# Performance work log

Hardware: AMD Instinct MI355X
Metric: run time of the kernel (lower is better)

Reference implementation:

```python
import jax, jax.numpy as jnp
import numpy as np

BS, NC, Nc, D_n = 8, 256, 128, 64
ALPHA, HS, HM = 2, 256, 128
GAMMA_MAX = 0.5
EPS = 1e-6


def setup_inputs() -> dict:
    key = jax.random.key(0)
    ks = jax.random.split(key, 12)
    f = jax.random.normal
    return {
        "x": f(ks[0], (BS, NC, D_n), jnp.float32),
        "h": f(ks[1], (BS, NC, Nc, D_n), jnp.float32) * 0.1,
        "W": f(ks[2], (BS, NC, Nc, Nc), jnp.float32) * (Nc ** -0.5),
        "decay": jax.random.uniform(ks[3], (BS, NC, Nc), jnp.float32),
        "hebbian": f(ks[4], (BS, NC, Nc, Nc), jnp.float32) * 0.01,
        "neuron_id": f(ks[5], (NC, Nc, D_n), jnp.float32) * (D_n ** -0.5),
        "state_w1": f(ks[6], (HS, 2 * D_n), jnp.float32) * ((2 * D_n) ** -0.5),
        "state_b1": jnp.zeros((HS,), jnp.float32),
        "state_w2": f(ks[7], (D_n, HS), jnp.float32) * (HS ** -0.5),
        "state_b2": jnp.zeros((D_n,), jnp.float32),
        "msg_w1": f(ks[8], (HM, D_n), jnp.float32) * (D_n ** -0.5),
        "msg_b1": jnp.zeros((HM,), jnp.float32),
        "msg_w2": f(ks[9], (D_n, HM), jnp.float32) * (HM ** -0.5),
        "msg_b2": jnp.zeros((D_n,), jnp.float32),
        "inject_w": f(ks[10], (NC, ALPHA * D_n, D_n), jnp.float32) * (D_n ** -0.5),
        "inject_b": jnp.zeros((NC, ALPHA * D_n), jnp.float32),
        "W_decay_logit": jnp.full((NC, Nc), -3.0, jnp.float32),
        "decay_gamma_logit": jnp.full((NC, Nc), -3.0, jnp.float32),
        "hebbian_decay_logit": jnp.full((NC, Nc), 2.0, jnp.float32),
    }


def _rms_norm(v):
    # F.rms_norm over the last (Nc) axis, no affine weight
    return v * jax.lax.rsqrt(jnp.mean(v * v, axis=-1, keepdims=True) + EPS)


def reference(x, h, W, decay, hebbian, neuron_id,
              state_w1, state_b1, state_w2, state_b2,
              msg_w1, msg_b1, msg_w2, msg_b2,
              inject_w, inject_b,
              W_decay_logit, decay_gamma_logit, hebbian_decay_logit):
    B = x.shape[0]
    # per-cell injection of external input into the first ALPHA neurons
    inj = jnp.einsum('bcd,cad->bca', x, inject_w) + inject_b   # [B,NC,ALPHA*D_n]
    h = h.at[:, :, :ALPHA, :].add(inj.reshape(B, NC, ALPHA, D_n))
    h_id = h + neuron_id                                       # identity embedding broadcast
    # per-neuron message MLP (tanh hidden)
    m = jnp.tanh(jnp.einsum('bcnd,hd->bcnh', h_id, msg_w1) + msg_b1)
    m = jnp.einsum('bcnh,dh->bcnd', m, msg_w2) + msg_b2        # [B,NC,Nc,D_n]
    # Hebbian-weighted adjacency message passing: small per-cell matmul W @ m
    agg = jnp.einsum('bcij,bcjd->bcid', W, m)
    # state update MLP on concat(state, aggregated message)
    s = jnp.tanh(jnp.einsum('bcnd,hd->bcnh',
                            jnp.concatenate([h_id, agg], axis=-1), state_w1) + state_b1)
    dh = jnp.einsum('bcnh,dh->bcnd', s, state_w2) + state_b2
    # gated decay of per-neuron state
    dg = GAMMA_MAX * jax.nn.sigmoid(decay_gamma_logit)         # [NC,Nc]
    decay_new = (1.0 - dg) * decay + dg * jax.nn.sigmoid(jnp.mean(dh, axis=-1))
    h_new = (1.0 - decay_new[..., None]) * h + decay_new[..., None] * jnp.tanh(dh)
    # Hebbian outer-product plasticity
    hg = GAMMA_MAX * jax.nn.sigmoid(hebbian_decay_logit)
    outer = jnp.einsum('bcid,bcjd->bcij', h_new, m) / D_n
    hebbian_new = (1.0 - hg[..., None]) * hebbian + hg[..., None] * outer
    # decayed adjacency update + rms-norm over the incoming-edge axis
    wg = GAMMA_MAX * jax.nn.sigmoid(W_decay_logit)
    W_new = _rms_norm((1.0 - wg[..., None]) * W + wg[..., None] * hebbian_new)
    return (h_new, m, W_new, decay_new, hebbian_new)
```

## Files before the change

### kernel.cpp

```cpp
#include <hip/hip_runtime.h>


#define NCELL 256

typedef __attribute__((ext_vector_type(8))) short bf16x8;
typedef __attribute__((ext_vector_type(4))) float f32x4;
typedef __attribute__((ext_vector_type(4))) unsigned short u16x4;

#define MFMA(a, b, c) __builtin_amdgcn_mfma_f32_16x16x32_bf16((a), (b), (c), 0, 0, 0)

__device__ __forceinline__ unsigned short f2bf(float f) {
    unsigned u = __builtin_bit_cast(unsigned, f);
    u = (u + 0x7FFFu + ((u >> 16) & 1u)) >> 16;
    return (unsigned short)u;
}
__device__ __forceinline__ float frcp(float x) { return __builtin_amdgcn_rcpf(x); }
__device__ __forceinline__ float sigm(float v) { return frcp(1.0f + __expf(-v)); }
__device__ __forceinline__ float ftanh(float x) {
    float e = __expf(2.0f * x);
    return 1.0f - 2.0f * frcp(e + 1.0f);
}

__device__ __forceinline__ int sw64(int row, int col) {
    return row * 64 + ((((col >> 3) ^ row) & 7) << 3) + (col & 7);
}
__device__ __forceinline__ int sw128(int row, int col) {
    return row * 128 + (((col >> 3) ^ (row & 7)) << 3) + (col & 7);
}
__device__ __forceinline__ int sw32(int row, int col) {
    return row * 32 + ((((col >> 3) ^ row) & 3) << 3) + (col & 7);
}

__global__ void cvt_w(const float* __restrict__ a, const float* __restrict__ b,
                      const float* __restrict__ c, const float* __restrict__ d,
                      unsigned short* __restrict__ dst) {
    int i = blockIdx.x * 256 + threadIdx.x;
    float v;
    if (i < 8192) v = a[i];
    else if (i < 16384) v = b[i - 8192];
    else if (i < 49152) v = c[i - 16384];
    else v = d[i - 49152];
    dst[i] = f2bf(v);
}

__global__ __launch_bounds__(256, 4)
void cell_kernel(const float* __restrict__ x, const float* __restrict__ h,
                 const float* __restrict__ W, const float* __restrict__ decay,
                 const float* __restrict__ nid,
                 const float* __restrict__ sb1, const float* __restrict__ sb2,
                 const float* __restrict__ mb1, const float* __restrict__ mb2,
                 const float* __restrict__ injw, const float* __restrict__ injb,
                 const float* __restrict__ dgl,
                 const unsigned short* __restrict__ wbf,
                 float* __restrict__ out) {
    const int cell = blockIdx.x;
    const int c = cell & (NCELL - 1);
    const int tid = threadIdx.x;
    const int wv = tid >> 6;
    const int lane = tid & 63;
    const int lr = lane & 15;
    const int lg = lane >> 4;

    float* out_h = out;
    float* out_m = out + 16777216;
    float* out_d = out + 67108864;

    const unsigned short* w1m = wbf;
    const unsigned short* w2m = wbf + 8192;
    const unsigned short* w1s = wbf + 16384;
    const unsigned short* w2s = wbf + 49152;

    __shared__ alignas(16) unsigned char smem[33280];
    unsigned short* mT_s = (unsigned short*)smem;
    unsigned short* st_s = (unsigned short*)(smem + 16384);
    float* inj_s = (float*)(smem + 32768);
    unsigned short* hbuf = st_s + wv * 2048;

    float4 wpa[4][2][2];
    {
        const float* Wbase = W + (size_t)cell * 16384;
        #pragma unroll
        for (int ks = 0; ks < 4; ++ks)
            #pragma unroll
            for (int rt = 0; rt < 2; ++rt) {
                const float* wr = Wbase + (wv * 32 + rt * 16 + lr) * 128 + ks * 32 + lg * 8;
                wpa[ks][rt][0] = *(const float4*)wr;
                wpa[ks][rt][1] = *(const float4*)(wr + 4);
            }
    }

    if (wv == 0) {
        const float* xr = x + cell * 64;
        const float* i0 = injw + (c * 128 + lane) * 64;
        const float* i1 = i0 + 64 * 64;
        float acc0 = injb[c * 128 + lane];
        float acc1 = injb[c * 128 + 64 + lane];
        #pragma unroll
        for (int d4 = 0; d4 < 16; ++d4) {
            float4 xv = ((const float4*)xr)[d4];
            float4 a = ((const float4*)i0)[d4];
            float4 b = ((const float4*)i1)[d4];
            acc0 += a.x * xv.x + a.y * xv.y + a.z * xv.z + a.w * xv.w;
            acc1 += b.x * xv.x + b.y * xv.y + b.z * xv.z + b.w * xv.w;
        }
        inj_s[lane] = acc0;
        inj_s[64 + lane] = acc1;
    }

    bf16x8 aH[2][2];
    #pragma unroll
    for (int rt = 0; rt < 2; ++rt)
        #pragma unroll
        for (int ks = 0; ks < 2; ++ks) {
            const int row = wv * 32 + rt * 16 + lr;
            const int col = ks * 32 + lg * 8;
            const float* hr = h + (size_t)(cell * 128 + row) * 64 + col;
            const float* nr = nid + (size_t)(c * 128 + row) * 64 + col;
            float4 a0 = *(const float4*)hr;
            float4 a1 = *(const float4*)(hr + 4);
            float4 n0 = *(const float4*)nr;
            float4 n1 = *(const float4*)(nr + 4);
            float v[8] = {a0.x, a0.y, a0.z, a0.w, a1.x, a1.y, a1.z, a1.w};
            float nn[8] = {n0.x, n0.y, n0.z, n0.w, n1.x, n1.y, n1.z, n1.w};
            unsigned short us[8];
            #pragma unroll
            for (int j = 0; j < 8; ++j) {
                float hv = v[j] + nn[j];
                if (row < 2) hv += inj_s[row * 64 + col + j];
                us[j] = f2bf(hv);
            }
            aH[rt][ks] = *(bf16x8*)us;
        }

    f32x4 accM[2][4];
    #pragma unroll
    for (int rt = 0; rt < 2; ++rt)
        #pragma unroll
        for (int dt = 0; dt < 4; ++dt)
            accM[rt][dt] = (f32x4){0.f, 0.f, 0.f, 0.f};

    #pragma unroll
    for (int ch = 0; ch < 4; ++ch) {
        f32x4 accH[2][2];
        #pragma unroll
        for (int rt = 0; rt < 2; ++rt)
            #pragma unroll
            for (int ht = 0; ht < 2; ++ht)
                accH[rt][ht] = (f32x4){0.f, 0.f, 0.f, 0.f};
        #pragma unroll
        for (int ks = 0; ks < 2; ++ks)
            #pragma unroll
            for (int ht = 0; ht < 2; ++ht) {
                bf16x8 bw = *(const bf16x8*)&w1m[(ch * 32 + ht * 16 + lr) * 64 + ks * 32 + lg * 8];
                #pragma unroll
                for (int rt = 0; rt < 2; ++rt)
                    accH[rt][ht] = MFMA(aH[rt][ks], bw, accH[rt][ht]);
            }
        #pragma unroll
        for (int rt = 0; rt < 2; ++rt)
            #pragma unroll
            for (int ht = 0; ht < 2; ++ht) {
                float b1v = mb1[ch * 32 + ht * 16 + lr];
                #pragma unroll
                for (int r = 0; r < 4; ++r) {
                    float t = ftanh(accH[rt][ht][r] + b1v);
                    hbuf[sw32(rt * 16 + lg * 4 + r, ht * 16 + lr)] = f2bf(t);
                }
            }
        #pragma unroll
        for (int rt = 0; rt < 2; ++rt) {
            bf16x8 aM = *(const bf16x8*)&hbuf[sw32(rt * 16 + lr, lg * 8)];
            #pragma unroll
            for (int dt = 0; dt < 4; ++dt) {
                bf16x8 bw = *(const bf16x8*)&w2m[(dt * 16 + lr) * 128 + ch * 32 + lg * 8];
                accM[rt][dt] = MFMA(aM, bw, accM[rt][dt]);
            }
        }
    }
    #pragma unroll
    for (int rt = 0; rt < 2; ++rt)
        #pragma unroll
        for (int dt = 0; dt < 4; ++dt) {
            float b2v = mb2[dt * 16 + lr];
            #pragma unroll
            for (int r = 0; r < 4; ++r) {
                float mv = accM[rt][dt][r] + b2v;
                int n = wv * 32 + rt * 16 + lg * 4 + r;
                int dcol = dt * 16 + lr;
                out_m[(size_t)(cell * 128 + n) * 64 + dcol] = mv;
                mT_s[sw128(dcol, n)] = f2bf(mv);
            }
        }
    __syncthreads();

    f32x4 accA[2][4];
    #pragma unroll
    for (int rt = 0; rt < 2; ++rt)
        #pragma unroll
        for (int dt = 0; dt < 4; ++dt)
            accA[rt][dt] = (f32x4){0.f, 0.f, 0.f, 0.f};
    #pragma unroll
    for (int ks = 0; ks < 4; ++ks)
        #pragma unroll
        for (int rt = 0; rt < 2; ++rt) {
            float4 wa = wpa[ks][rt][0];
            float4 wb = wpa[ks][rt][1];
            unsigned short uw[8] = {f2bf(wa.x), f2bf(wa.y), f2bf(wa.z), f2bf(wa.w),
                                    f2bf(wb.x), f2bf(wb.y), f2bf(wb.z), f2bf(wb.w)};
            bf16x8 aW = *(bf16x8*)uw;
            #pragma unroll
            for (int dt = 0; dt < 4; ++dt) {
                bf16x8 bm = *(const bf16x8*)&mT_s[sw128(dt * 16 + lr, ks * 32 + lg * 8)];
                accA[rt][dt] = MFMA(aW, bm, accA[rt][dt]);
            }
        }
    #pragma unroll
    for (int rt = 0; rt < 2; ++rt)
        #pragma unroll
        for (int dt = 0; dt < 4; ++dt)
            #pragma unroll
            for (int r = 0; r < 4; ++r)
                st_s[sw64(wv * 32 + rt * 16 + lg * 4 + r, dt * 16 + lr)] = f2bf(accA[rt][dt][r]);

    bf16x8 aG[2][2];
    #pragma unroll
    for (int rt = 0; rt < 2; ++rt)
        #pragma unroll
        for (int ks = 0; ks < 2; ++ks)
            aG[rt][ks] = *(const bf16x8*)&st_s[sw64(wv * 32 + rt * 16 + lr, ks * 32 + lg * 8)];

    f32x4 accD[2][4];
    #pragma unroll
    for (int rt = 0; rt < 2; ++rt)
        #pragma unroll
        for (int dt = 0; dt < 4; ++dt)
            accD[rt][dt] = (f32x4){0.f, 0.f, 0.f, 0.f};

    #pragma unroll
    for (int ch = 0; ch < 8; ++ch) {
        f32x4 accS[2][2];
        #pragma unroll
        for (int rt = 0; rt < 2; ++rt)
            #pragma unroll
            for (int ht = 0; ht < 2; ++ht)
                accS[rt][ht] = (f32x4){0.f, 0.f, 0.f, 0.f};
        #pragma unroll
        for (int ks = 0; ks < 4; ++ks)
            #pragma unroll
            for (int ht = 0; ht < 2; ++ht) {
                bf16x8 bw = *(const bf16x8*)&w1s[(ch * 32 + ht * 16 + lr) * 128 + ks * 32 + lg * 8];
                #pragma unroll
                for (int rt = 0; rt < 2; ++rt) {
                    bf16x8 af = (ks < 2) ? aH[rt][ks] : aG[rt][ks - 2];
                    accS[rt][ht] = MFMA(af, bw, accS[rt][ht]);
                }
            }
        #pragma unroll
        for (int rt = 0; rt < 2; ++rt)
            #pragma unroll
            for (int ht = 0; ht < 2; ++ht) {
                float bv = sb1[ch * 32 + ht * 16 + lr];
                #pragma unroll
                for (int r = 0; r < 4; ++r) {
                    float t = ftanh(accS[rt][ht][r] + bv);
                    hbuf[sw32(rt * 16 + lg * 4 + r, ht * 16 + lr)] = f2bf(t);
                }
            }
        #pragma unroll
        for (int rt = 0; rt < 2; ++rt) {
            bf16x8 aS = *(const bf16x8*)&hbuf[sw32(rt * 16 + lr, lg * 8)];
            #pragma unroll
            for (int dt = 0; dt < 4; ++dt) {
                bf16x8 bw = *(const bf16x8*)&w2s[(dt * 16 + lr) * 256 + ch * 32 + lg * 8];
                accD[rt][dt] = MFMA(aS, bw, accD[rt][dt]);
            }
        }
    }

    float dnew_r[2][4];
    #pragma unroll
    for (int rt = 0; rt < 2; ++rt)
        #pragma unroll
        for (int r = 0; r < 4; ++r) {
            float s = 0.f;
            #pragma unroll
            for (int dt = 0; dt < 4; ++dt) {
                accD[rt][dt][r] += sb2[dt * 16 + lr];
                s += accD[rt][dt][r];
            }
            s += __shfl_xor(s, 1);
            s += __shfl_xor(s, 2);
            s += __shfl_xor(s, 4);
            s += __shfl_xor(s, 8);
            int row = wv * 32 + rt * 16 + lg * 4 + r;
            float mean = s * (1.0f / 64.0f);
            float dg = 0.5f * sigm(dgl[c * 128 + row]);
            float dn = (1.0f - dg) * decay[cell * 128 + row] + dg * sigm(mean);
            if (lr == 0) out_d[cell * 128 + row] = dn;
            dnew_r[rt][r] = dn;
        }
    #pragma unroll
    for (int rt = 0; rt < 2; ++rt)
        #pragma unroll
        for (int r = 0; r < 4; ++r) {
            int row = wv * 32 + rt * 16 + lg * 4 + r;
            float dn = dnew_r[rt][r];
            const float* hr = h + (size_t)(cell * 128 + row) * 64;
            #pragma unroll
            for (int dt = 0; dt < 4; ++dt) {
                int col = dt * 16 + lr;
                float hpost = hr[col];
                if (row < 2) hpost += inj_s[row * 64 + col];
                float hn = (1.0f - dn) * hpost + dn * ftanh(accD[rt][dt][r]);
                out_h[(size_t)(cell * 128 + row) * 64 + col] = hn;
            }
        }
}

__global__ __launch_bounds__(256, 4)
void hebb_kernel(const float* __restrict__ W, const float* __restrict__ hebb,
                 const float* __restrict__ wdl, const float* __restrict__ hdl,
                 float* __restrict__ out) {
    const int cell = blockIdx.x;
    const int c = cell & (NCELL - 1);
    const int tid = threadIdx.x;
    const int wv = tid >> 6;
    const int lane = tid & 63;
    const int lr = lane & 15;
    const int lg = lane >> 4;

    const float* hsrc = out + (size_t)cell * 8192;
    const float* msrc = out + 16777216 + (size_t)cell * 8192;
    float* out_W  = out + 33554432;
    float* out_hb = out + 67371008;

    __shared__ alignas(16) unsigned char smem[32768];
    unsigned short* hA = (unsigned short*)smem;
    unsigned short* mB = (unsigned short*)(smem + 16384);

    #pragma unroll
    for (int g = 0; g < 8; ++g) {
        int idx = g * 1024 + tid * 4;
        int row = idx >> 6, col = idx & 63;
        float4 hv = *(const float4*)(hsrc + idx);
        float4 mv = *(const float4*)(msrc + idx);
        u16x4 hu = {f2bf(hv.x), f2bf(hv.y), f2bf(hv.z), f2bf(hv.w)};
        u16x4 mu = {f2bf(mv.x), f2bf(mv.y), f2bf(mv.z), f2bf(mv.w)};
        *(u16x4*)&hA[sw64(row, col)] = hu;
        *(u16x4*)&mB[sw64(row, col)] = mu;
    }
    __syncthreads();

    bf16x8 aO[2][2];
    #pragma unroll
    for (int rt = 0; rt < 2; ++rt)
        #pragma unroll
        for (int ks = 0; ks < 2; ++ks)
            aO[rt][ks] = *(const bf16x8*)&hA[sw64(wv * 32 + rt * 16 + lr, ks * 32 + lg * 8)];

    f32x4 accO[2][8];
    #pragma unroll
    for (int rt = 0; rt < 2; ++rt)
        #pragma unroll
        for (int jt = 0; jt < 8; ++jt)
            accO[rt][jt] = (f32x4){0.f, 0.f, 0.f, 0.f};
    #pragma unroll
    for (int jt = 0; jt < 8; ++jt)
        #pragma unroll
        for (int ks = 0; ks < 2; ++ks) {
            bf16x8 bm = *(const bf16x8*)&mB[sw64(jt * 16 + lr, ks * 32 + lg * 8)];
            #pragma unroll
            for (int rt = 0; rt < 2; ++rt)
                accO[rt][jt] = MFMA(aO[rt][ks], bm, accO[rt][jt]);
        }

    #pragma unroll
    for (int rt = 0; rt < 2; ++rt)
        #pragma unroll
        for (int r = 0; r < 4; ++r) {
            int i = wv * 32 + rt * 16 + lg * 4 + r;
            float hg = 0.5f * sigm(hdl[c * 128 + i]);
            float wg = 0.5f * sigm(wdl[c * 128 + i]);
            const float* hbr = hebb + (size_t)(cell * 128 + i) * 128;
            const float* Wr = W + (size_t)(cell * 128 + i) * 128;
            float* ohb = out_hb + (size_t)(cell * 128 + i) * 128;
            float wpre[8];
            float ss = 0.f;
            #pragma unroll
            for (int jt = 0; jt < 8; ++jt) {
                int j = jt * 16 + lr;
                float o = accO[rt][jt][r] * (1.0f / 64.0f);
                float hbn = (1.0f - hg) * hbr[j] + hg * o;
                ohb[j] = hbn;
                float wp = (1.0f - wg) * Wr[j] + wg * hbn;
                wpre[jt] = wp;
                ss += wp * wp;
            }
            ss += __shfl_xor(ss, 1);
            ss += __shfl_xor(ss, 2);
            ss += __shfl_xor(ss, 4);
            ss += __shfl_xor(ss, 8);
            float scale = rsqrtf(ss * (1.0f / 128.0f) + 1e-6f);
            float* oW = out_W + (size_t)(cell * 128 + i) * 128;
            #pragma unroll
            for (int jt = 0; jt < 8; ++jt)
                oW[jt * 16 + lr] = wpre[jt] * scale;
        }
}

extern "C" void kernel_launch(void* const* d_in, const int* in_sizes, int n_in,
                              void* d_out, int out_size, void* d_ws, size_t ws_size,
                              hipStream_t stream) {
    const float* x    = (const float*)d_in[0];
    const float* h    = (const float*)d_in[1];
    const float* W    = (const float*)d_in[2];
    const float* dec  = (const float*)d_in[3];
    const float* hebb = (const float*)d_in[4];
    const float* nid  = (const float*)d_in[5];
    const float* sw1  = (const float*)d_in[6];
    const float* sb1  = (const float*)d_in[7];
    const float* sw2  = (const float*)d_in[8];
    const float* sb2  = (const float*)d_in[9];
    const float* mw1  = (const float*)d_in[10];
    const float* mb1  = (const float*)d_in[11];
    const float* mw2  = (const float*)d_in[12];
    const float* mb2  = (const float*)d_in[13];
    const float* injw = (const float*)d_in[14];
    const float* injb = (const float*)d_in[15];
    const float* wdl  = (const float*)d_in[16];
    const float* dgl  = (const float*)d_in[17];
    const float* hdl  = (const float*)d_in[18];

    unsigned short* wbf = (unsigned short*)d_ws;

    cvt_w<<<256, 256, 0, stream>>>(mw1, mw2, sw1, sw2, wbf);
    cell_kernel<<<2048, 256, 0, stream>>>(x, h, W, dec, nid, sb1, sb2, mb1, mb2,
                                          injw, injb, dgl, wbf, (float*)d_out);
    hebb_kernel<<<2048, 256, 0, stream>>>(W, hebb, wdl, hdl, (float*)d_out);
}
```

Measured before the change: 376.0 us.

## Cut registers and LDS to raise occupancy in cell kernel

Stops prefetching the W tile into registers at kernel start and loads it right before the W@m matmul. The st_s scratch now aliases mT_s behind an added barrier, and the per-wave hbuf shrinks, reducing LDS use. It also limits unrolling of the MLP chunk loops, raises launch bounds to 6 blocks per CU, and swaps the manual bf16 rounding for the library conversion. The aim is higher occupancy to hide latency, at the cost of exposing the W load latency, adding an extra sync, and possible spills under the tighter register budget.

```diff
diff --git a/kernel.cpp b/kernel.cpp
--- a/kernel.cpp
+++ b/kernel.cpp
@@ -1,4 +1,5 @@
 #include <hip/hip_runtime.h>
+#include <hip/hip_bf16.h>
 
 
 #define NCELL 256
@@ -10,9 +11,7 @@
 #define MFMA(a, b, c) __builtin_amdgcn_mfma_f32_16x16x32_bf16((a), (b), (c), 0, 0, 0)
 
 __device__ __forceinline__ unsigned short f2bf(float f) {
-    unsigned u = __builtin_bit_cast(unsigned, f);
-    u = (u + 0x7FFFu + ((u >> 16) & 1u)) >> 16;
-    return (unsigned short)u;
+    return __builtin_bit_cast(unsigned short, __float2bfloat16(f));
 }
 __device__ __forceinline__ float frcp(float x) { return __builtin_amdgcn_rcpf(x); }
 __device__ __forceinline__ float sigm(float v) { return frcp(1.0f + __expf(-v)); }
@@ -43,7 +42,7 @@
     dst[i] = f2bf(v);
 }
 
-__global__ __launch_bounds__(256, 4)
+__global__ __launch_bounds__(256, 6)
 void cell_kernel(const float* __restrict__ x, const float* __restrict__ h,
                  const float* __restrict__ W, const float* __restrict__ decay,
                  const float* __restrict__ nid,
@@ -70,24 +69,11 @@
     const unsigned short* w1s = wbf + 16384;
     const unsigned short* w2s = wbf + 49152;
 
-    __shared__ alignas(16) unsigned char smem[33280];
-    unsigned short* mT_s = (unsigned short*)smem;
-    unsigned short* st_s = (unsigned short*)(smem + 16384);
-    float* inj_s = (float*)(smem + 32768);
-    unsigned short* hbuf = st_s + wv * 2048;
-
-    float4 wpa[4][2][2];
-    {
-        const float* Wbase = W + (size_t)cell * 16384;
-        #pragma unroll
-        for (int ks = 0; ks < 4; ++ks)
-            #pragma unroll
-            for (int rt = 0; rt < 2; ++rt) {
-                const float* wr = Wbase + (wv * 32 + rt * 16 + lr) * 128 + ks * 32 + lg * 8;
-                wpa[ks][rt][0] = *(const float4*)wr;
-                wpa[ks][rt][1] = *(const float4*)(wr + 4);
-            }
-    }
+    __shared__ alignas(16) unsigned short mT_s[8192];
+    __shared__ alignas(16) unsigned short hbuf_all[4096];
+    __shared__ float inj_s[128];
+    unsigned short* hbuf = hbuf_all + wv * 1024;
+    unsigned short* st_s = mT_s;
 
     if (wv == 0) {
         const float* xr = x + cell * 64;
@@ -139,7 +125,7 @@
         for (int dt = 0; dt < 4; ++dt)
             accM[rt][dt] = (f32x4){0.f, 0.f, 0.f, 0.f};
 
-    #pragma unroll
+    #pragma unroll 2
     for (int ch = 0; ch < 4; ++ch) {
         f32x4 accH[2][2];
         #pragma unroll
@@ -199,21 +185,27 @@
         #pragma unroll
         for (int dt = 0; dt < 4; ++dt)
             accA[rt][dt] = (f32x4){0.f, 0.f, 0.f, 0.f};
-    #pragma unroll
-    for (int ks = 0; ks < 4; ++ks)
-        #pragma unroll
-        for (int rt = 0; rt < 2; ++rt) {
-            float4 wa = wpa[ks][rt][0];
-            float4 wb = wpa[ks][rt][1];
-            unsigned short uw[8] = {f2bf(wa.x), f2bf(wa.y), f2bf(wa.z), f2bf(wa.w),
-                                    f2bf(wb.x), f2bf(wb.y), f2bf(wb.z), f2bf(wb.w)};
-            bf16x8 aW = *(bf16x8*)uw;
-            #pragma unroll
-            for (int dt = 0; dt < 4; ++dt) {
-                bf16x8 bm = *(const bf16x8*)&mT_s[sw128(dt * 16 + lr, ks * 32 + lg * 8)];
-                accA[rt][dt] = MFMA(aW, bm, accA[rt][dt]);
-            }
-        }
+    {
+        const float* Wbase = W + (size_t)cell * 16384;
+        #pragma unroll
+        for (int ks = 0; ks < 4; ++ks)
+            #pragma unroll
+            for (int rt = 0; rt < 2; ++rt) {
+                const float* wr = Wbase + (wv * 32 + rt * 16 + lr) * 128 + ks * 32 + lg * 8;
+                float4 wa = *(const float4*)wr;
+                float4 wb = *(const float4*)(wr + 4);
+                unsigned short uw[8] = {f2bf(wa.x), f2bf(wa.y), f2bf(wa.z), f2bf(wa.w),
+                                        f2bf(wb.x), f2bf(wb.y), f2bf(wb.z), f2bf(wb.w)};
+                bf16x8 aW = *(bf16x8*)uw;
+                #pragma unroll
+                for (int dt = 0; dt < 4; ++dt) {
+                    bf16x8 bm = *(const bf16x8*)&mT_s[sw128(dt * 16 + lr, ks * 32 + lg * 8)];
+                    accA[rt][dt] = MFMA(aW, bm, accA[rt][dt]);
+                }
+            }
+    }
+    __syncthreads();
+
     #pragma unroll
     for (int rt = 0; rt < 2; ++rt)
         #pragma unroll
@@ -236,7 +228,7 @@
         for (int dt = 0; dt < 4; ++dt)
             accD[rt][dt] = (f32x4){0.f, 0.f, 0.f, 0.f};
 
-    #pragma unroll
+    #pragma unroll 2
     for (int ch = 0; ch < 8; ++ch) {
         f32x4 accS[2][2];
         #pragma unroll
```

Measured after the change: 768.8 us. 104% more time.
